# Kernel optimization log

Measured on AMD Instinct MI355X. Metric: run time of the kernel, lower is better.

## Reference

```python
import jax, jax.numpy as jnp
import numpy as np

B, S, D = 2, 2048, 2048
H, HD = 16, 128
WINDOW = 512
ROPE_BASE = 10000.0


def setup_inputs() -> dict:
    key = jax.random.key(0)
    k1, k2, k3 = jax.random.split(key, 3)
    x = jax.random.normal(k1, (B, S, D), dtype=jnp.float32)
    w_qkv = jax.random.normal(k2, (3 * D, D), dtype=jnp.float32) * (D ** -0.5)
    w_out = jax.random.normal(k3, (D, D), dtype=jnp.float32) * (D ** -0.5)
    return {"x": x, "w_qkv": w_qkv, "w_out": w_out}


def _rope_cos_sin(seq_len, head_dim, base, dtype):
    inv_freq = 1.0 / (base ** (jnp.arange(0, head_dim, 2, dtype=jnp.float32) / head_dim))
    pos = jnp.arange(seq_len, dtype=jnp.float32)
    freqs = pos[:, None] * inv_freq[None, :]            # (S, HD/2)
    emb = jnp.concatenate([freqs, freqs], axis=-1)       # (S, HD)
    return jnp.cos(emb).astype(dtype), jnp.sin(emb).astype(dtype)


def _rotate_half(x):
    x1, x2 = jnp.split(x, 2, axis=-1)
    return jnp.concatenate([-x2, x1], axis=-1)


def reference(x, w_qkv, w_out):
    Bx, Sx, Dx = x.shape
    # fused QKV projection (torch Linear: x @ W^T)
    qkv = jnp.einsum('bsd,ed->bse', x, w_qkv)
    q, k, v = jnp.split(qkv, 3, axis=-1)
    q = q.reshape(Bx, Sx, H, HD).transpose(0, 2, 1, 3)   # (B,H,S,HD)
    k = k.reshape(Bx, Sx, H, HD).transpose(0, 2, 1, 3)
    v = v.reshape(Bx, Sx, H, HD).transpose(0, 2, 1, 3)
    # RoPE with implicit position_ids = arange(S)
    cos, sin = _rope_cos_sin(Sx, HD, ROPE_BASE, x.dtype)  # (S, HD)
    q = q * cos[None, None] + _rotate_half(q) * sin[None, None]
    k = k * cos[None, None] + _rotate_half(k) * sin[None, None]
    # sliding-window attention: attend iff 0 <= i - j < WINDOW
    scale = 1.0 / jnp.sqrt(jnp.array(HD, dtype=x.dtype))
    scores = jnp.einsum('bhqd,bhkd->bhqk', q, k) * scale
    i = jnp.arange(Sx)[:, None]
    j = jnp.arange(Sx)[None, :]
    diff = i - j
    valid = (diff >= 0) & (diff < WINDOW)                # (S, S)
    scores = jnp.where(valid[None, None], scores, jnp.finfo(scores.dtype).min)
    attn = jax.nn.softmax(scores, axis=-1)
    out = jnp.einsum('bhqk,bhkd->bhqd', attn, v)
    out = out.transpose(0, 2, 1, 3).reshape(Bx, Sx, Dx)
    return jnp.einsum('bsd,ed->bse', out, w_out)
```

## Files before the change

### kernel.cpp

```cpp
#include <hip/hip_runtime.h>

#define S_LEN 2048
#define DIM 2048
#define NH 16
#define HD 128
#define WIN 512
#define QKVD (3 * DIM)

typedef unsigned short u16;
typedef unsigned int u32;
typedef __bf16 bf16x8 __attribute__((ext_vector_type(8)));
typedef float f32x4 __attribute__((ext_vector_type(4)));

__device__ __forceinline__ u16 f2bf(float f) {
  unsigned u = __builtin_bit_cast(unsigned, f);
  u += 0x7FFFu + ((u >> 16) & 1u);
  return (u16)(u >> 16);
}
__device__ __forceinline__ float bf2f(u16 b) {
  return __builtin_bit_cast(float, (unsigned)b << 16);
}
__device__ __forceinline__ void async16(const void* g, void* l) {
  __builtin_amdgcn_global_load_lds((__attribute__((address_space(1))) void*)g,
                                   (__attribute__((address_space(3))) void*)l,
                                   16, 0, 0);
}
#define WAITV6 asm volatile("s_waitcnt vmcnt(6)" ::: "memory")

__global__ __launch_bounds__(256) void cvt_kernel(const float* __restrict__ in,
                                                  u16* __restrict__ out, int n) {
  int i = (blockIdx.x * 256 + threadIdx.x) * 4;
  if (i < n) {
    float4 v = *(const float4*)(in + i);
    ushort4 o;
    o.x = f2bf(v.x); o.y = f2bf(v.y); o.z = f2bf(v.z); o.w = f2bf(v.w);
    *(ushort4*)(out + i) = o;
  }
}

__global__ __launch_bounds__(256) void rope_tab_kernel(float* __restrict__ cosT,
                                                       float* __restrict__ sinT) {
  int idx = blockIdx.x * 256 + threadIdx.x;
  int s = idx >> 6, j = idx & 63;
  double freq = exp((double)j * -0.14391156831212787);
  double a = (double)s * freq;
  cosT[idx] = (float)cos(a);
  sinT[idx] = (float)sin(a);
}

__global__ __launch_bounds__(512, 2) void gemm8(const u16* __restrict__ A,
                                                const u16* __restrict__ B,
                                                u16* __restrict__ C,
                                                int M, int N, int K) {
  constexpr int ABY = 256 * 128;
  __shared__ __align__(16) char Al[2 * ABY];
  __shared__ __align__(16) char Bl[2 * ABY];

  const int tiles_n = N >> 8;
  const int nwg = gridDim.x;
  const int wg = ((int)blockIdx.x & 7) * (nwg >> 3) + ((int)blockIdx.x >> 3);
  const int m0 = (wg / tiles_n) << 8;
  const int n0 = (wg % tiles_n) << 8;
  const int t = threadIdx.x;
  const int l = t & 63, w = t >> 6;
  const int wr = w >> 2, wc = w & 3;
  const int l16 = l & 15, lg = l >> 4;
  const u16* Asrc = A + (size_t)m0 * K;
  const u16* Bsrc = B + (size_t)n0 * K;

  auto stA = [&](int kcol, int half, int b) {
#pragma unroll
    for (int j = 0; j < 2; ++j) {
      int c = t + j * 512;
      int rih = c >> 3, ch = c & 7;
      int row = (rih & 63) | ((rih >> 6) << 7) | (half << 6);
      async16(Asrc + (size_t)row * K + kcol + ((ch ^ (row & 7)) << 3),
              Al + b * ABY + row * 128 + ch * 16);
    }
  };
  auto stB = [&](int kcol, int half, int b) {
#pragma unroll
    for (int j = 0; j < 2; ++j) {
      int c = t + j * 512;
      int rih = c >> 3, ch = c & 7;
      int row = (rih & 31) | ((rih >> 5) << 6) | (half << 5);
      async16(Bsrc + (size_t)row * K + kcol + ((ch ^ (row & 7)) << 3),
              Bl + b * ABY + row * 128 + ch * 16);
    }
  };

  f32x4 acc[8][4] = {};
  bf16x8 af[4][2];
  bf16x8 bfr[2][2][2];

  auto rdA = [&](int b, int mh) {
#pragma unroll
    for (int m = 0; m < 4; ++m)
#pragma unroll
      for (int ks = 0; ks < 2; ++ks) {
        int row = wr * 128 + mh * 64 + m * 16 + l16;
        int ch = ks * 4 + lg;
        af[m][ks] = *(const bf16x8*)(Al + b * ABY + row * 128 + ((ch ^ (row & 7)) << 4));
      }
  };
  auto rdB = [&](int b, int nh) {
#pragma unroll
    for (int n = 0; n < 2; ++n)
#pragma unroll
      for (int ks = 0; ks < 2; ++ks) {
        int row = wc * 64 + nh * 32 + n * 16 + l16;
        int ch = ks * 4 + lg;
        bfr[nh][n][ks] = *(const bf16x8*)(Bl + b * ABY + row * 128 + ((ch ^ (row & 7)) << 4));
      }
  };
  auto mm = [&](int mh, int nh) {
#pragma unroll
    for (int m = 0; m < 4; ++m)
#pragma unroll
      for (int n = 0; n < 2; ++n)
#pragma unroll
        for (int ks = 0; ks < 2; ++ks)
          acc[mh * 4 + m][nh * 2 + n] = __builtin_amdgcn_mfma_f32_16x16x32_bf16(
              af[m][ks], bfr[nh][n][ks], acc[mh * 4 + m][nh * 2 + n], 0, 0, 0);
  };

  const int NT = K >> 6;
  stA(0, 0, 0); stB(0, 0, 0); stB(0, 1, 0); stA(0, 1, 0); stA(64, 0, 1);
  WAITV6;
  __builtin_amdgcn_s_barrier();

  for (int kt = 0; kt < NT; ++kt) {
    const int b = kt & 1, nb = b ^ 1;
    const int k1 = ((kt + 1 < NT) ? kt + 1 : kt) << 6;
    const int k2 = ((kt + 2 < NT) ? kt + 2 : kt) << 6;
    rdA(b, 0); rdB(b, 0);
    stB(k1, 0, nb);
    __builtin_amdgcn_s_barrier();
    __builtin_amdgcn_s_setprio(1); mm(0, 0); __builtin_amdgcn_s_setprio(0);
    WAITV6;
    __builtin_amdgcn_s_barrier();
    rdB(b, 1);
    stB(k1, 1, nb);
    __builtin_amdgcn_s_barrier();
    __builtin_amdgcn_s_setprio(1); mm(0, 1); __builtin_amdgcn_s_setprio(0);
    WAITV6;
    __builtin_amdgcn_s_barrier();
    rdA(b, 1);
    stA(k1, 1, nb);
    __builtin_amdgcn_s_barrier();
    __builtin_amdgcn_s_setprio(1); mm(1, 0); __builtin_amdgcn_s_setprio(0);
    __builtin_amdgcn_s_barrier();
    stA(k2, 0, b);
    __builtin_amdgcn_s_barrier();
    __builtin_amdgcn_s_setprio(1); mm(1, 1); __builtin_amdgcn_s_setprio(0);
    WAITV6;
    __builtin_amdgcn_s_barrier();
  }

  const int rb = m0 + wr * 128 + lg * 4;
  const int cb = n0 + wc * 64 + l16;
#pragma unroll
  for (int mi = 0; mi < 8; ++mi)
#pragma unroll
    for (int ni = 0; ni < 4; ++ni)
#pragma unroll
      for (int r = 0; r < 4; ++r)
        C[(size_t)(rb + mi * 16 + r) * N + cb + ni * 16] = f2bf(acc[mi][ni][r]);
}

template <typename TO>
__global__ __launch_bounds__(256, 2) void gemm_bt(const u16* __restrict__ A,
                                                  const u16* __restrict__ B,
                                                  TO* __restrict__ C,
                                                  int M, int N, int K) {
  __shared__ __align__(16) u16 As[128 * 64];
  __shared__ __align__(16) u16 Bs[128 * 64];
  const int tiles_n = N >> 7;
  const int m0 = (blockIdx.x / tiles_n) << 7;
  const int n0 = (blockIdx.x % tiles_n) << 7;
  const int t = threadIdx.x;
  const int l = t & 63, w = t >> 6;
  const int wr = w >> 1, wc = w & 1;
  const int l16 = l & 15, lg = l >> 4;
  f32x4 acc[4][4] = {};
  for (int k0 = 0; k0 < K; k0 += 64) {
    __syncthreads();
#pragma unroll
    for (int i = 0; i < 4; ++i) {
      int c = t + (i << 8);
      int r = c >> 3, cc = c & 7;
      async16(A + (size_t)(m0 + r) * K + k0 + cc * 8, (char*)As + c * 16);
    }
#pragma unroll
    for (int i = 0; i < 4; ++i) {
      int c = t + (i << 8);
      int r = c >> 3, cc = c & 7;
      async16(B + (size_t)(n0 + r) * K + k0 + cc * 8, (char*)Bs + c * 16);
    }
    __syncthreads();
#pragma unroll
    for (int ks = 0; ks < 2; ++ks) {
      bf16x8 af[4], bfv[4];
#pragma unroll
      for (int m = 0; m < 4; ++m)
        af[m] = *(const bf16x8*)(As + (wr * 64 + m * 16 + l16) * 64 + ks * 32 + lg * 8);
#pragma unroll
      for (int n = 0; n < 4; ++n)
        bfv[n] = *(const bf16x8*)(Bs + (wc * 64 + n * 16 + l16) * 64 + ks * 32 + lg * 8);
#pragma unroll
      for (int m = 0; m < 4; ++m)
#pragma unroll
        for (int n = 0; n < 4; ++n)
          acc[m][n] = __builtin_amdgcn_mfma_f32_16x16x32_bf16(af[m], bfv[n], acc[m][n], 0, 0, 0);
    }
  }
  const int rb = m0 + wr * 64 + lg * 4;
  const int cb = n0 + wc * 64 + l16;
#pragma unroll
  for (int m = 0; m < 4; ++m)
#pragma unroll
    for (int n = 0; n < 4; ++n)
#pragma unroll
      for (int r = 0; r < 4; ++r) {
        float v = acc[m][n][r];
        size_t idx = (size_t)(rb + m * 16 + r) * N + cb + n * 16;
        if constexpr (sizeof(TO) == 2) C[idx] = f2bf(v);
        else C[idx] = v;
      }
}

__global__ __launch_bounds__(256) void rope_kernel(u16* __restrict__ qkv,
                                                   const float* __restrict__ cosT,
                                                   const float* __restrict__ sinT) {
  const int row = blockIdx.x;
  const int s = row & (S_LEN - 1);
  const int t = threadIdx.x;
  u16* base = qkv + (size_t)row * QKVD;
#pragma unroll
  for (int j = 0; j < 4; ++j) {
    const int pi = t + j * 256;
    const int h = pi >> 6, d = pi & 63;
    const float c = cosT[(s << 6) + d];
    const float sn = sinT[(s << 6) + d];
    u16* q = base + h * HD;
    float q1 = bf2f(q[d]), q2 = bf2f(q[d + 64]);
    q[d] = f2bf(q1 * c - q2 * sn);
    q[d + 64] = f2bf(q2 * c + q1 * sn);
    u16* k = base + DIM + h * HD;
    float k1 = bf2f(k[d]), k2 = bf2f(k[d + 64]);
    k[d] = f2bf(k1 * c - k2 * sn);
    k[d + 64] = f2bf(k2 * c + k1 * sn);
  }
}

__global__ __launch_bounds__(512, 3) void attn_kernel(const u16* __restrict__ qkv,
                                                      u16* __restrict__ attnO) {
  const int bid = blockIdx.x;
  const int qt = bid & 15;
  const int bh = bid >> 4;
  const int q0 = qt << 7;
  const int b = bh >> 4, h = bh & 15;
  const u16* Qp = qkv + (size_t)b * S_LEN * QKVD + h * HD;
  const u16* Kp = Qp + DIM;
  const u16* Vp = Qp + 2 * DIM;
  __shared__ __align__(16) char Ks[64 * 256];
  __shared__ __align__(16) u16 Vt[128][72];
  __shared__ __align__(16) u32 Ps[8][16 * 36];
  const int t = threadIdx.x;
  const int w = t >> 6, l = t & 63;
  const int l16 = l & 15, lg = l >> 4;
  const int q0w = q0 + w * 16;
  const bf16x8 ones = __builtin_bit_cast(bf16x8,
      (uint4){0x3F803F80u, 0x3F803F80u, 0x3F803F80u, 0x3F803F80u});
  bf16x8 qf[4];
  {
    const u16* qrow = Qp + (size_t)(q0w + l16) * QKVD;
#pragma unroll
    for (int ks = 0; ks < 4; ++ks) qf[ks] = *(const bf16x8*)(qrow + ks * 32 + lg * 8);
  }
  f32x4 oacc[8] = {};
  f32x4 ldacc = {};
  const int lo = max(0, (q0 - (WIN - 1)) >> 6);
  const int hi = (q0 + 127) >> 6;
  const int lo_w = max(0, (q0w - (WIN - 1)) >> 6);
  const int hi_w = (q0w + 15) >> 6;
  const float SC2 = 0.12751744654f;
  const int qi = q0w + l16;
  for (int kt = lo; kt <= hi; ++kt) {
    const int kv0 = kt << 6;
    __syncthreads();
#pragma unroll
    for (int i = 0; i < 2; ++i) {
      int c = t + (i << 9);
      int row = c >> 4, ch = c & 15;
      int sch = ch ^ (row & 7);
      async16(Kp + (size_t)(kv0 + row) * QKVD + sch * 8, Ks + c * 16);
    }
    {
      const int dc = t & 15, pp = t >> 4;
      const int kv = pp * 2, d0 = dc * 8;
      const uint4 va = *(const uint4*)(Vp + (size_t)(kv0 + kv) * QKVD + d0);
      const uint4 vb = *(const uint4*)(Vp + (size_t)(kv0 + kv + 1) * QKVD + d0);
      unsigned av[4] = {va.x, va.y, va.z, va.w};
      unsigned bv[4] = {vb.x, vb.y, vb.z, vb.w};
#pragma unroll
      for (int j = 0; j < 4; ++j) {
        *(unsigned*)&Vt[d0 + j * 2][kv] = (av[j] & 0xffffu) | (bv[j] << 16);
        *(unsigned*)&Vt[d0 + j * 2 + 1][kv] = (av[j] >> 16) | (bv[j] & 0xffff0000u);
      }
    }
    __syncthreads();
    if (kt < lo_w || kt > hi_w) continue;
    u32* pbase = &Ps[w][0];
#pragma unroll
    for (int c4 = 0; c4 < 4; ++c4) {
      f32x4 sa = {};
#pragma unroll
      for (int ks = 0; ks < 4; ++ks) {
        const int krow = c4 * 16 + l16;
        const int ch = (ks * 4 + lg) ^ (krow & 7);
        bf16x8 kf = *(const bf16x8*)(Ks + krow * 256 + ch * 16);
        sa = __builtin_amdgcn_mfma_f32_16x16x32_bf16(kf, qf[ks], sa, 0, 0, 0);
      }
      const int kj_base = kv0 + c4 * 16 + lg * 4;
      float p[4];
#pragma unroll
      for (int r = 0; r < 4; ++r) {
        unsigned diff = (unsigned)(qi - (kj_base + r));
        float v = sa[r] * SC2;
        v = (diff < WIN) ? v : -1e30f;
        p[r] = __builtin_amdgcn_exp2f(v);
      }
      const u32 w0 = (u32)f2bf(p[0]) | ((u32)f2bf(p[1]) << 16);
      const u32 w1 = (u32)f2bf(p[2]) | ((u32)f2bf(p[3]) << 16);
      const int pw = l16 * 36 + c4 * 8 + lg * 2;
      pbase[pw] = w0;
      pbase[pw + 1] = w1;
    }
    asm volatile("s_waitcnt lgkmcnt(0)" ::: "memory");
    __builtin_amdgcn_sched_barrier(0);
#pragma unroll
    for (int ks = 0; ks < 2; ++ks) {
      uint4 pr = *(const uint4*)&Ps[w][l16 * 36 + ks * 16 + lg * 4];
      bf16x8 pf = __builtin_bit_cast(bf16x8, pr);
#pragma unroll
      for (int dt = 0; dt < 8; ++dt) {
        bf16x8 vf = *(const bf16x8*)(&Vt[dt * 16 + l16][ks * 32 + lg * 8]);
        oacc[dt] = __builtin_amdgcn_mfma_f32_16x16x32_bf16(pf, vf, oacc[dt], 0, 0, 0);
      }
      ldacc = __builtin_amdgcn_mfma_f32_16x16x32_bf16(pf, ones, ldacc, 0, 0, 0);
    }
  }
  const int qr = q0w + lg * 4;
  u16* orow = attnO + ((size_t)(b * S_LEN + qr) * DIM) + h * HD;
#pragma unroll
  for (int r = 0; r < 4; ++r) {
    float inv = 1.f / ldacc[r];
#pragma unroll
    for (int dt = 0; dt < 8; ++dt)
      orow[(size_t)r * DIM + dt * 16 + l16] = f2bf(oacc[dt][r] * inv);
  }
}

extern "C" void kernel_launch(void* const* d_in, const int* in_sizes, int n_in,
                              void* d_out, int out_size, void* d_ws, size_t ws_size,
                              hipStream_t stream) {
  const float* x = (const float*)d_in[0];
  const float* w_qkv = (const float*)d_in[1];
  const float* w_out = (const float*)d_in[2];
  float* out = (float*)d_out;

  char* ws = (char*)d_ws;
  size_t off = 0;
  auto alloc = [&](size_t bytes) {
    void* p = ws + off;
    off = (off + bytes + 255) & ~(size_t)255;
    return p;
  };
  const size_t rows = 2ull * S_LEN;
  u16* wqkvb = (u16*)alloc(3ull * DIM * DIM * 2);
  u16* woutb = (u16*)alloc((size_t)DIM * DIM * 2);
  u16* xb    = (u16*)alloc(rows * DIM * 2);
  u16* qkvb  = (u16*)alloc(rows * 3 * DIM * 2);
  float* cosT = (float*)alloc((size_t)S_LEN * 64 * 4);
  float* sinT = (float*)alloc((size_t)S_LEN * 64 * 4);

  cvt_kernel<<<(3 * DIM * DIM) / 1024, 256, 0, stream>>>(w_qkv, wqkvb, 3 * DIM * DIM);
  cvt_kernel<<<(DIM * DIM) / 1024, 256, 0, stream>>>(w_out, woutb, DIM * DIM);
  cvt_kernel<<<(int)(rows * DIM / 1024), 256, 0, stream>>>(x, xb, (int)(rows * DIM));
  rope_tab_kernel<<<(S_LEN * 64) / 256, 256, 0, stream>>>(cosT, sinT);
  gemm8<<<(int)(rows / 256) * (QKVD / 256), 512, 0, stream>>>(
      xb, wqkvb, qkvb, (int)rows, QKVD, DIM);
  rope_kernel<<<(int)rows, 256, 0, stream>>>(qkvb, cosT, sinT);
  u16* attnb = wqkvb;
  attn_kernel<<<2 * NH * (S_LEN / 128), 512, 0, stream>>>(qkvb, attnb);
  gemm_bt<float><<<(int)(rows / 128) * (DIM / 128), 256, 0, stream>>>(
      attnb, woutb, out, (int)rows, DIM, DIM);
}
```

Before: 253.1 us.

## Merge conversion kernels, remap out-proj blocks across XCDs, vectorize RoPE

The three fp32-to-bf16 conversion launches become one kernel that picks its source and destination by element range, saving two launches. The output-projection GEMM remaps block IDs so that consecutive tiles land on the same XCD, which should improve L2 reuse of shared A/B tiles. The RoPE kernel now has each thread handle 8 contiguous bf16 values with 16-byte loads and stores and vector cos/sin reads, replacing scattered 2-byte accesses. The block remap assumes the grid size is divisible by 8.

```diff
diff --git a/kernel.cpp b/kernel.cpp
--- a/kernel.cpp
+++ b/kernel.cpp
@@ -27,15 +27,21 @@
 }
 #define WAITV6 asm volatile("s_waitcnt vmcnt(6)" ::: "memory")
 
-__global__ __launch_bounds__(256) void cvt_kernel(const float* __restrict__ in,
-                                                  u16* __restrict__ out, int n) {
+__global__ __launch_bounds__(256) void cvt3_kernel(
+    const float* __restrict__ a, u16* __restrict__ oa, int na,
+    const float* __restrict__ b, u16* __restrict__ ob, int nb,
+    const float* __restrict__ c, u16* __restrict__ oc, int nc) {
   int i = (blockIdx.x * 256 + threadIdx.x) * 4;
-  if (i < n) {
-    float4 v = *(const float4*)(in + i);
-    ushort4 o;
-    o.x = f2bf(v.x); o.y = f2bf(v.y); o.z = f2bf(v.z); o.w = f2bf(v.w);
-    *(ushort4*)(out + i) = o;
-  }
+  const float* src;
+  u16* dst;
+  if (i < na) { src = a + i; dst = oa + i; }
+  else if (i < na + nb) { src = b + (i - na); dst = ob + (i - na); }
+  else if (i < na + nb + nc) { src = c + (i - na - nb); dst = oc + (i - na - nb); }
+  else return;
+  float4 v = *(const float4*)src;
+  ushort4 o;
+  o.x = f2bf(v.x); o.y = f2bf(v.y); o.z = f2bf(v.z); o.w = f2bf(v.w);
+  *(ushort4*)dst = o;
 }
 
 __global__ __launch_bounds__(256) void rope_tab_kernel(float* __restrict__ cosT,
@@ -176,8 +182,10 @@
   __shared__ __align__(16) u16 As[128 * 64];
   __shared__ __align__(16) u16 Bs[128 * 64];
   const int tiles_n = N >> 7;
-  const int m0 = (blockIdx.x / tiles_n) << 7;
-  const int n0 = (blockIdx.x % tiles_n) << 7;
+  const int nwg = gridDim.x;
+  const int wg = ((int)blockIdx.x & 7) * (nwg >> 3) + ((int)blockIdx.x >> 3);
+  const int m0 = (wg / tiles_n) << 7;
+  const int n0 = (wg % tiles_n) << 7;
   const int t = threadIdx.x;
   const int l = t & 63, w = t >> 6;
   const int wr = w >> 1, wc = w & 1;
@@ -235,22 +243,32 @@
   const int row = blockIdx.x;
   const int s = row & (S_LEN - 1);
   const int t = threadIdx.x;
-  u16* base = qkv + (size_t)row * QKVD;
+  const int part = t >> 7;
+  const int h = (t >> 3) & 15;
+  const int c = t & 7;
+  u16* p = qkv + (size_t)row * QKVD + part * DIM + h * HD + c * 8;
+  const float* cp = cosT + (s << 6) + c * 8;
+  const float* sp = sinT + (s << 6) + c * 8;
+  const float4 c0 = *(const float4*)cp, c1 = *(const float4*)(cp + 4);
+  const float4 s0 = *(const float4*)sp, s1 = *(const float4*)(sp + 4);
+  float cs[8] = {c0.x, c0.y, c0.z, c0.w, c1.x, c1.y, c1.z, c1.w};
+  float sn[8] = {s0.x, s0.y, s0.z, s0.w, s1.x, s1.y, s1.z, s1.w};
+  uint4 lo = *(const uint4*)p;
+  uint4 hi = *(const uint4*)(p + 64);
+  unsigned lw[4] = {lo.x, lo.y, lo.z, lo.w};
+  unsigned hw[4] = {hi.x, hi.y, hi.z, hi.w};
+  unsigned ol[4], oh[4];
 #pragma unroll
   for (int j = 0; j < 4; ++j) {
-    const int pi = t + j * 256;
-    const int h = pi >> 6, d = pi & 63;
-    const float c = cosT[(s << 6) + d];
-    const float sn = sinT[(s << 6) + d];
-    u16* q = base + h * HD;
-    float q1 = bf2f(q[d]), q2 = bf2f(q[d + 64]);
-    q[d] = f2bf(q1 * c - q2 * sn);
-    q[d + 64] = f2bf(q2 * c + q1 * sn);
-    u16* k = base + DIM + h * HD;
-    float k1 = bf2f(k[d]), k2 = bf2f(k[d + 64]);
-    k[d] = f2bf(k1 * c - k2 * sn);
-    k[d + 64] = f2bf(k2 * c + k1 * sn);
-  }
+    float x1a = bf2f((u16)(lw[j] & 0xffffu)), x1b = bf2f((u16)(lw[j] >> 16));
+    float x2a = bf2f((u16)(hw[j] & 0xffffu)), x2b = bf2f((u16)(hw[j] >> 16));
+    float ca = cs[j * 2], cb = cs[j * 2 + 1];
+    float sa = sn[j * 2], sb = sn[j * 2 + 1];
+    ol[j] = (u32)f2bf(x1a * ca - x2a * sa) | ((u32)f2bf(x1b * cb - x2b * sb) << 16);
+    oh[j] = (u32)f2bf(x2a * ca + x1a * sa) | ((u32)f2bf(x2b * cb + x1b * sb) << 16);
+  }
+  *(uint4*)p = (uint4){ol[0], ol[1], ol[2], ol[3]};
+  *(uint4*)(p + 64) = (uint4){oh[0], oh[1], oh[2], oh[3]};
 }
 
 __global__ __launch_bounds__(512, 3) void attn_kernel(const u16* __restrict__ qkv,
@@ -385,9 +403,10 @@
   float* cosT = (float*)alloc((size_t)S_LEN * 64 * 4);
   float* sinT = (float*)alloc((size_t)S_LEN * 64 * 4);
 
-  cvt_kernel<<<(3 * DIM * DIM) / 1024, 256, 0, stream>>>(w_qkv, wqkvb, 3 * DIM * DIM);
-  cvt_kernel<<<(DIM * DIM) / 1024, 256, 0, stream>>>(w_out, woutb, DIM * DIM);
-  cvt_kernel<<<(int)(rows * DIM / 1024), 256, 0, stream>>>(x, xb, (int)(rows * DIM));
+  const int na = 3 * DIM * DIM, nb = DIM * DIM, nc = (int)(rows * DIM);
+  cvt3_kernel<<<(na + nb + nc) / 1024, 256, 0, stream>>>(w_qkv, wqkvb, na,
+                                                         w_out, woutb, nb,
+                                                         x, xb, nc);
   rope_tab_kernel<<<(S_LEN * 64) / 256, 256, 0, stream>>>(cosT, sinT);
   gemm8<<<(int)(rows / 256) * (QKVD / 256), 512, 0, stream>>>(
       xb, wqkvb, qkvb, (int)rows, QKVD, DIM);
```

Result: no change. 251.4 us (-0.7%).
